# Kernel tuning notes

Hardware: AMD Instinct MI355X
Metric: run time of the kernel (lower is better)

Reference implementation:

```python
import jax, jax.numpy as jnp
import numpy as np

HEADS = 16

def split_heads(v, heads):
    # NOTE: faithful to the source: reshape [B,S,D] -> [B,S,h_dim,heads], then
    # transpose to [B,heads,S,h_dim]. This interleaves channels across heads
    # (different from the standard [B,S,heads,h_dim] split).
    B, S, D = v.shape
    hd = D // heads
    return v.reshape(B, S, hd, heads).transpose(0, 3, 1, 2)

def merge_heads(v):
    # [B,heads,S,h_dim] -> transpose [B,S,h_dim,heads] -> reshape [B,S,D]
    B, H, S, hd = v.shape
    return v.transpose(0, 2, 3, 1).reshape(B, S, H * hd)

def setup_inputs() -> dict:
    key = jax.random.key(0)
    ks = jax.random.split(key, 5)
    B, S, D = 2, 2048, 1024
    return {
        "x": jax.random.normal(ks[0], (B, S, D), dtype=jnp.float32),
        "qw": jax.random.normal(ks[1], (D, D), dtype=jnp.float32),
        "kw": jax.random.normal(ks[2], (D, D), dtype=jnp.float32),
        "vw": jax.random.normal(ks[3], (D, D), dtype=jnp.float32),
        "ow": jax.random.normal(ks[4], (D, D), dtype=jnp.float32),
    }

def reference(x, qw, kw, vw, ow):
    B, S, D = x.shape
    Q = split_heads(x @ qw, HEADS)  # [B,H,S,hd]
    K = split_heads(x @ kw, HEADS)
    V = split_heads(x @ vw, HEADS)
    # NOTE: scale is 1/sqrt(dim), NOT 1/sqrt(head_dim), as in the source.
    scale = 1.0 / jnp.sqrt(jnp.float32(D))
    score = jnp.einsum("bhqd,bhkd->bhqk", Q, K) * scale  # [B,H,S,S]
    causal = jnp.tril(jnp.ones((1, 1, S, S), dtype=score.dtype))
    score = score - 1e10 * (1.0 - causal)
    weights = jax.nn.softmax(score, axis=-1)
    attn = jnp.einsum("bhqk,bhkd->bhqd", weights, V)
    return merge_heads(attn) @ ow
```

## Files before the change

kernel.cpp:

```cpp
#include <hip/hip_runtime.h>


typedef __bf16 bf16x8 __attribute__((ext_vector_type(8)));
typedef float  f32x4  __attribute__((ext_vector_type(4)));

#define S_LEN  2048
#define DMODEL 1024
#define NHEADS 16
#define HDIM   64
#define LOG2E  1.44269504088896340736f

__device__ __forceinline__ void gll16(const __bf16* g, __bf16* l) {
    __builtin_amdgcn_global_load_lds(
        (const __attribute__((address_space(1))) unsigned int*)g,
        (__attribute__((address_space(3))) unsigned int*)l, 16, 0, 0);
}

__global__ __launch_bounds__(256) void prep_all(
    const float* __restrict__ x,
    const float* __restrict__ qw, const float* __restrict__ kw,
    const float* __restrict__ vw, const float* __restrict__ ow,
    __bf16* __restrict__ xhi, __bf16* __restrict__ xlo,
    __bf16* __restrict__ qwthi, __bf16* __restrict__ qwtlo,
    __bf16* __restrict__ kwthi, __bf16* __restrict__ kwtlo,
    __bf16* __restrict__ vwt,  __bf16* __restrict__ owt) {
    __shared__ float tile[32][33];
    int id = blockIdx.x;
    if (id < 4096) {
        int i = id * 256 + threadIdx.x;
        float4 v = ((const float4*)x)[i];
        __bf16 h0 = (__bf16)v.x, h1 = (__bf16)v.y, h2 = (__bf16)v.z, h3 = (__bf16)v.w;
        ushort4 hh, ll;
        hh.x = __builtin_bit_cast(unsigned short, h0);
        hh.y = __builtin_bit_cast(unsigned short, h1);
        hh.z = __builtin_bit_cast(unsigned short, h2);
        hh.w = __builtin_bit_cast(unsigned short, h3);
        ll.x = __builtin_bit_cast(unsigned short, (__bf16)(v.x - (float)h0));
        ll.y = __builtin_bit_cast(unsigned short, (__bf16)(v.y - (float)h1));
        ll.z = __builtin_bit_cast(unsigned short, (__bf16)(v.z - (float)h2));
        ll.w = __builtin_bit_cast(unsigned short, (__bf16)(v.w - (float)h3));
        ((ushort4*)xhi)[i] = hh;
        ((ushort4*)xlo)[i] = ll;
        return;
    }
    int rid = id - 4096;
    int z = rid >> 10;
    int bx = rid & 31, by = (rid >> 5) & 31;
    const float* w = (z == 0) ? qw : (z == 1) ? kw : (z == 2) ? vw : ow;
    int n0 = bx * 32, k0 = by * 32;
    int tx = threadIdx.x & 31, ty = threadIdx.x >> 5;
#pragma unroll
    for (int i = 0; i < 32; i += 8)
        tile[ty + i][tx] = w[(k0 + ty + i) * DMODEL + n0 + tx];
    __syncthreads();
#pragma unroll
    for (int i = 0; i < 32; i += 8) {
        float f = tile[tx][ty + i];
        int k = k0 + tx, n = n0 + ty + i;
        if (z <= 1) {
            __bf16 fh = (__bf16)f;
            __bf16 fl = (__bf16)(f - (float)fh);
            int c = (n & 15) * 64 + (n >> 4);
            if (z == 0) { qwthi[c * DMODEL + k] = fh; qwtlo[c * DMODEL + k] = fl; }
            else        { kwthi[c * DMODEL + k] = fh; kwtlo[c * DMODEL + k] = fl; }
        } else if (z == 2) {
            vwt[n * DMODEL + k] = (__bf16)f;
        } else {
            int ck = (k & 15) * 64 + (k >> 4);
            owt[n * DMODEL + ck] = (__bf16)f;
        }
    }
}

__global__ __launch_bounds__(256) void qkv_gemm(
    const __bf16* __restrict__ xhi, const __bf16* __restrict__ xlo,
    const __bf16* __restrict__ qwthi, const __bf16* __restrict__ qwtlo,
    const __bf16* __restrict__ kwthi, const __bf16* __restrict__ kwtlo,
    const __bf16* __restrict__ vwt,
    __bf16* __restrict__ Qhi, __bf16* __restrict__ Qlo,
    __bf16* __restrict__ Khi, __bf16* __restrict__ Klo,
    __bf16* __restrict__ Vt) {
    __shared__ __bf16 Ash[128][32], Asl[128][32], Bsh[128][32], Bsl[128][32];
    int mode = blockIdx.z;
    int tid  = threadIdx.x;
    int wave = tid >> 6, lane = tid & 63;
    int quad = lane >> 4, l15 = lane & 15;
    int wm = (wave >> 1) * 64, wn = (wave & 1) * 64;
    int grow = lane >> 2;
    int gcol = (((lane & 3) - ((lane >> 3) & 3)) & 3) * 8;
    int sA   = ((quad + (l15 >> 1)) & 3) * 8;
    const int K = DMODEL;

    if (mode < 2) {
        const __bf16* Bh = mode ? kwthi : qwthi;
        const __bf16* Bl = mode ? kwtlo : qwtlo;
        int m0 = blockIdx.y * 128, n0 = blockIdx.x * 128;
        f32x4 acc[4][4] = {};
        for (int k0 = 0; k0 < K; k0 += 32) {
            __syncthreads();
#pragma unroll
            for (int ps = 0; ps < 2; ps++) {
                int row = ps * 64 + wave * 16;
                gll16(&xhi[(m0 + row + grow) * K + k0 + gcol], &Ash[row][0]);
                gll16(&xlo[(m0 + row + grow) * K + k0 + gcol], &Asl[row][0]);
                gll16(&Bh [(n0 + row + grow) * K + k0 + gcol], &Bsh[row][0]);
                gll16(&Bl [(n0 + row + grow) * K + k0 + gcol], &Bsl[row][0]);
            }
            __syncthreads();
            bf16x8 ah[4], al[4], bh[4], bl[4];
#pragma unroll
            for (int mi = 0; mi < 4; mi++) {
                ah[mi] = *(const bf16x8*)&Ash[wm + mi * 16 + l15][sA];
                al[mi] = *(const bf16x8*)&Asl[wm + mi * 16 + l15][sA];
            }
#pragma unroll
            for (int ni = 0; ni < 4; ni++) {
                bh[ni] = *(const bf16x8*)&Bsh[wn + ni * 16 + l15][sA];
                bl[ni] = *(const bf16x8*)&Bsl[wn + ni * 16 + l15][sA];
            }
#pragma unroll
            for (int mi = 0; mi < 4; mi++)
#pragma unroll
                for (int ni = 0; ni < 4; ni++) {
                    acc[mi][ni] = __builtin_amdgcn_mfma_f32_16x16x32_bf16(ah[mi], bh[ni], acc[mi][ni], 0, 0, 0);
                    acc[mi][ni] = __builtin_amdgcn_mfma_f32_16x16x32_bf16(ah[mi], bl[ni], acc[mi][ni], 0, 0, 0);
                    acc[mi][ni] = __builtin_amdgcn_mfma_f32_16x16x32_bf16(al[mi], bh[ni], acc[mi][ni], 0, 0, 0);
                }
        }
        float oscale = mode ? 1.0f : 0.03125f * LOG2E;
        __bf16* Ohi = mode ? Khi : Qhi;
        __bf16* Olo = mode ? Klo : Qlo;
#pragma unroll
        for (int mi = 0; mi < 4; mi++)
#pragma unroll
            for (int ni = 0; ni < 4; ni++)
#pragma unroll
                for (int rg = 0; rg < 4; rg++) {
                    int m = m0 + wm + mi * 16 + quad * 4 + rg;
                    int n = n0 + wn + ni * 16 + l15;
                    float v = acc[mi][ni][rg] * oscale;
                    size_t idx = (size_t)m * DMODEL + n;
                    __bf16 vh = (__bf16)v;
                    Ohi[idx] = vh;
                    Olo[idx] = (__bf16)(v - (float)vh);
                }
    } else {
        int ch0 = blockIdx.x * 128, xm0 = blockIdx.y * 128;
        f32x4 acc[4][4] = {};
        for (int k0 = 0; k0 < K; k0 += 32) {
            __syncthreads();
#pragma unroll
            for (int ps = 0; ps < 2; ps++) {
                int row = ps * 64 + wave * 16;
                gll16(&vwt[(ch0 + row + grow) * K + k0 + gcol], &Ash[row][0]);
                gll16(&xhi[(xm0 + row + grow) * K + k0 + gcol], &Bsh[row][0]);
            }
            __syncthreads();
            bf16x8 af[4], bfr[4];
#pragma unroll
            for (int mi = 0; mi < 4; mi++)
                af[mi] = *(const bf16x8*)&Ash[wm + mi * 16 + l15][sA];
#pragma unroll
            for (int ni = 0; ni < 4; ni++)
                bfr[ni] = *(const bf16x8*)&Bsh[wn + ni * 16 + l15][sA];
#pragma unroll
            for (int mi = 0; mi < 4; mi++)
#pragma unroll
                for (int ni = 0; ni < 4; ni++)
                    acc[mi][ni] = __builtin_amdgcn_mfma_f32_16x16x32_bf16(
                        af[mi], bfr[ni], acc[mi][ni], 0, 0, 0);
        }
#pragma unroll
        for (int mi = 0; mi < 4; mi++)
#pragma unroll
            for (int ni = 0; ni < 4; ni++)
#pragma unroll
                for (int rg = 0; rg < 4; rg++) {
                    int ch = ch0 + wm + mi * 16 + quad * 4 + rg;
                    int xm = xm0 + wn + ni * 16 + l15;
                    int b = xm >> 11, s = xm & 2047;
                    int h = ch & 15,  d = ch >> 4;
                    Vt[((size_t)(b * NHEADS + h) * HDIM + d) * S_LEN + s] =
                        (__bf16)acc[mi][ni][rg];
                }
    }
}

__global__ __launch_bounds__(256) void out_gemm(const __bf16* __restrict__ A,
                                                const __bf16* __restrict__ Bt,
                                                float* __restrict__ out) {
    __shared__ __bf16 As[64][32];
    __shared__ __bf16 Bs[128][32];
    int tid  = threadIdx.x;
    int wave = tid >> 6, lane = tid & 63;
    int quad = lane >> 4, l15 = lane & 15;
    int m0 = blockIdx.y * 64, n0 = blockIdx.x * 128;
    int wm = (wave >> 1) * 32, wn = (wave & 1) * 64;
    int grow = lane >> 2;
    int gcol = (((lane & 3) - ((lane >> 3) & 3)) & 3) * 8;
    int sA   = ((quad + (l15 >> 1)) & 3) * 8;
    const int K = DMODEL;
    f32x4 acc[2][4] = {};

    for (int k0 = 0; k0 < K; k0 += 32) {
        __syncthreads();
        gll16(&A[(m0 + wave * 16 + grow) * K + k0 + gcol], &As[wave * 16][0]);
#pragma unroll
        for (int ps = 0; ps < 2; ps++) {
            int row = ps * 64 + wave * 16;
            gll16(&Bt[(n0 + row + grow) * K + k0 + gcol], &Bs[row][0]);
        }
        __syncthreads();
        bf16x8 af[2], bfr[4];
#pragma unroll
        for (int mi = 0; mi < 2; mi++)
            af[mi] = *(const bf16x8*)&As[wm + mi * 16 + l15][sA];
#pragma unroll
        for (int ni = 0; ni < 4; ni++)
            bfr[ni] = *(const bf16x8*)&Bs[wn + ni * 16 + l15][sA];
#pragma unroll
        for (int mi = 0; mi < 2; mi++)
#pragma unroll
            for (int ni = 0; ni < 4; ni++)
                acc[mi][ni] = __builtin_amdgcn_mfma_f32_16x16x32_bf16(
                    af[mi], bfr[ni], acc[mi][ni], 0, 0, 0);
    }

#pragma unroll
    for (int mi = 0; mi < 2; mi++)
#pragma unroll
        for (int ni = 0; ni < 4; ni++)
#pragma unroll
            for (int rg = 0; rg < 4; rg++) {
                int m = m0 + wm + mi * 16 + quad * 4 + rg;
                int n = n0 + wn + ni * 16 + l15;
                out[(size_t)m * DMODEL + n] = acc[mi][ni][rg];
            }
}

__global__ __launch_bounds__(256, 2) void flash_attn(const __bf16* __restrict__ Qhi,
                                                     const __bf16* __restrict__ Qlo,
                                                     const __bf16* __restrict__ Khi,
                                                     const __bf16* __restrict__ Klo,
                                                     const __bf16* __restrict__ Vt,
                                                     __bf16* __restrict__ attn) {
    int id  = blockIdx.x;
    int xcd = id & 7, r = id >> 3;
    int bh  = xcd + 8 * (r & 3);
    int rr  = r >> 2;
    int t   = (rr < 8) ? (15 - rr) : (rr - 8);
    int b = bh >> 4, h = bh & 15;
    const __bf16* Qh_hi = Qhi + (size_t)b * S_LEN * DMODEL + h * HDIM;
    const __bf16* Qh_lo = Qlo + (size_t)b * S_LEN * DMODEL + h * HDIM;
    const __bf16* Kh_hi = Khi + (size_t)b * S_LEN * DMODEL + h * HDIM;
    const __bf16* Kh_lo = Klo + (size_t)b * S_LEN * DMODEL + h * HDIM;
    const __bf16* Vh    = Vt  + (size_t)bh * HDIM * S_LEN;

    int tid = threadIdx.x, wave = tid >> 6, lane = tid & 63;
    int quad = lane >> 4, l15 = lane & 15;
    int iters = 2 * t + 2;

    __shared__ __bf16 KhF[8 * 64 * 8];
    __shared__ __bf16 KlF[8 * 64 * 8];
    __shared__ __bf16 VF [8 * 64 * 8];
    __shared__ __bf16 Ps[4][32][72];

    int c1  = tid >> 6, key = tid & 63;
    int inner = (c1 * 16 + (key & 15)) * 8;
    int rK    = (key >> 4);
    int kdst0 = rK * 512 + inner, kdst1 = (4 + rK) * 512 + inner;
    const __bf16* vrow = Vh + (size_t)key * S_LEN;

    int qbase = t * 128 + wave * 32;
    bf16x8 aqh0[2], aqh1[2], aql0[2], aql1[2];
#pragma unroll
    for (int qh = 0; qh < 2; qh++) {
        size_t qr = (size_t)(qbase + qh * 16 + l15) * DMODEL;
        aqh0[qh] = *(const bf16x8*)&Qh_hi[qr + quad * 8];
        aqh1[qh] = *(const bf16x8*)&Qh_hi[qr + 32 + quad * 8];
        aql0[qh] = *(const bf16x8*)&Qh_lo[qr + quad * 8];
        aql1[qh] = *(const bf16x8*)&Qh_lo[qr + 32 + quad * 8];
    }

    bf16x8 ones;
#pragma unroll
    for (int j = 0; j < 8; j++) ones[j] = (__bf16)1.0f;

    uint4 pk0, pk1, pl0, pl1, pv0, pv1;
    {
        const __bf16* sk = Kh_hi + (size_t)key * DMODEL;
        const __bf16* sl = Kh_lo + (size_t)key * DMODEL;
        pk0 = *(const uint4*)(sk + c1 * 8); pk1 = *(const uint4*)(sk + c1 * 8 + 32);
        pl0 = *(const uint4*)(sl + c1 * 8); pl1 = *(const uint4*)(sl + c1 * 8 + 32);
        pv0 = *(const uint4*)(vrow + c1 * 8); pv1 = *(const uint4*)(vrow + c1 * 8 + 32);
    }

    float m[2][4] = {{-3e38f, -3e38f, -3e38f, -3e38f},
                     {-3e38f, -3e38f, -3e38f, -3e38f}};
    f32x4 o[2][4] = {};
    f32x4 ol[2] = {};

    for (int i = 0; i < iters; i++) {
        int key0 = i * 64;

        __syncthreads();
        *(uint4*)&KhF[kdst0] = pk0;  *(uint4*)&KhF[kdst1] = pk1;
        *(uint4*)&KlF[kdst0] = pl0;  *(uint4*)&KlF[kdst1] = pl1;
        *(uint4*)&VF [kdst0] = pv0;  *(uint4*)&VF [kdst1] = pv1;
        __syncthreads();

        if (i + 1 < iters) {
            int key0n = (i + 1) * 64;
            const __bf16* sk = Kh_hi + (size_t)(key0n + key) * DMODEL;
            const __bf16* sl = Kh_lo + (size_t)(key0n + key) * DMODEL;
            pk0 = *(const uint4*)(sk + c1 * 8); pk1 = *(const uint4*)(sk + c1 * 8 + 32);
            pl0 = *(const uint4*)(sl + c1 * 8); pl1 = *(const uint4*)(sl + c1 * 8 + 32);
            pv0 = *(const uint4*)(vrow + key0n + c1 * 8);
            pv1 = *(const uint4*)(vrow + key0n + c1 * 8 + 32);
        }

        if (key0 > qbase + 31) continue;

        f32x4 sc[2][4] = {};
#pragma unroll
        for (int ni = 0; ni < 4; ni++) {
            bf16x8 kh0 = *(const bf16x8*)&KhF[(ni * 64 + lane) * 8];
            bf16x8 kh1 = *(const bf16x8*)&KhF[((4 + ni) * 64 + lane) * 8];
            bf16x8 kl0 = *(const bf16x8*)&KlF[(ni * 64 + lane) * 8];
            bf16x8 kl1 = *(const bf16x8*)&KlF[((4 + ni) * 64 + lane) * 8];
#pragma unroll
            for (int qh = 0; qh < 2; qh++) {
                sc[qh][ni] = __builtin_amdgcn_mfma_f32_16x16x32_bf16(aqh0[qh], kh0, sc[qh][ni], 0, 0, 0);
                sc[qh][ni] = __builtin_amdgcn_mfma_f32_16x16x32_bf16(aqh1[qh], kh1, sc[qh][ni], 0, 0, 0);
                sc[qh][ni] = __builtin_amdgcn_mfma_f32_16x16x32_bf16(aqh0[qh], kl0, sc[qh][ni], 0, 0, 0);
                sc[qh][ni] = __builtin_amdgcn_mfma_f32_16x16x32_bf16(aqh1[qh], kl1, sc[qh][ni], 0, 0, 0);
                sc[qh][ni] = __builtin_amdgcn_mfma_f32_16x16x32_bf16(aql0[qh], kh0, sc[qh][ni], 0, 0, 0);
                sc[qh][ni] = __builtin_amdgcn_mfma_f32_16x16x32_bf16(aql1[qh], kh1, sc[qh][ni], 0, 0, 0);
            }
        }

        if (i >= 2 * t) {
#pragma unroll
            for (int qh = 0; qh < 2; qh++) {
                int qrb = qbase + qh * 16 + quad * 4;
#pragma unroll
                for (int ni = 0; ni < 4; ni++) {
                    int keyi = key0 + ni * 16 + l15;
#pragma unroll
                    for (int rg = 0; rg < 4; rg++)
                        if (keyi > qrb + rg) sc[qh][ni][rg] = -1e30f;
                }
            }
        }

#pragma unroll
        for (int qh = 0; qh < 2; qh++) {
#pragma unroll
            for (int rg = 0; rg < 4; rg++) {
                float mx = fmaxf(fmaxf(sc[qh][0][rg], sc[qh][1][rg]),
                                 fmaxf(sc[qh][2][rg], sc[qh][3][rg]));
#pragma unroll
                for (int mm = 1; mm < 16; mm <<= 1)
                    mx = fmaxf(mx, __shfl_xor(mx, mm, 64));
                float mnew  = fmaxf(m[qh][rg], mx);
                float alpha = __builtin_amdgcn_exp2f(m[qh][rg] - mnew);
                m[qh][rg] = mnew;
#pragma unroll
                for (int ni = 0; ni < 4; ni++) {
                    float px = __builtin_amdgcn_exp2f(sc[qh][ni][rg] - mnew);
                    Ps[wave][qh * 16 + quad * 4 + rg][ni * 16 + l15] = (__bf16)px;
                }
                ol[qh][rg] *= alpha;
#pragma unroll
                for (int ni = 0; ni < 4; ni++)
                    o[qh][ni][rg] *= alpha;
            }
        }

#pragma unroll
        for (int step = 0; step < 2; step++) {
            bf16x8 ap0 = *(const bf16x8*)&Ps[wave][l15][step * 32 + quad * 8];
            bf16x8 ap1 = *(const bf16x8*)&Ps[wave][16 + l15][step * 32 + quad * 8];
            ol[0] = __builtin_amdgcn_mfma_f32_16x16x32_bf16(ap0, ones, ol[0], 0, 0, 0);
            ol[1] = __builtin_amdgcn_mfma_f32_16x16x32_bf16(ap1, ones, ol[1], 0, 0, 0);
#pragma unroll
            for (int ni = 0; ni < 4; ni++) {
                bf16x8 bv = *(const bf16x8*)&VF[((step * 4 + ni) * 64 + lane) * 8];
                o[0][ni] = __builtin_amdgcn_mfma_f32_16x16x32_bf16(ap0, bv, o[0][ni], 0, 0, 0);
                o[1][ni] = __builtin_amdgcn_mfma_f32_16x16x32_bf16(ap1, bv, o[1][ni], 0, 0, 0);
            }
        }
    }

#pragma unroll
    for (int qh = 0; qh < 2; qh++)
#pragma unroll
        for (int rg = 0; rg < 4; rg++) {
            float inv = 1.0f / ol[qh][rg];
            int q = qbase + qh * 16 + quad * 4 + rg;
#pragma unroll
            for (int ni = 0; ni < 4; ni++) {
                attn[((size_t)b * S_LEN + q) * DMODEL + h * HDIM + ni * 16 + l15] =
                    (__bf16)(o[qh][ni][rg] * inv);
            }
        }
}

extern "C" void kernel_launch(void* const* d_in, const int* in_sizes, int n_in,
                              void* d_out, int out_size, void* d_ws, size_t ws_size,
                              hipStream_t stream) {
    const float* x  = (const float*)d_in[0];
    const float* qw = (const float*)d_in[1];
    const float* kw = (const float*)d_in[2];
    const float* vw = (const float*)d_in[3];
    const float* ow = (const float*)d_in[4];

    char* ws = (char*)d_ws;
    const size_t MB = 1024 * 1024;
    __bf16* xhi   = (__bf16*)(ws);
    __bf16* xlo   = (__bf16*)(ws + 8 * MB);
    __bf16* qwthi = (__bf16*)(ws + 16 * MB);
    __bf16* qwtlo = (__bf16*)(ws + 18 * MB);
    __bf16* kwthi = (__bf16*)(ws + 20 * MB);
    __bf16* kwtlo = (__bf16*)(ws + 22 * MB);
    __bf16* vwt   = (__bf16*)(ws + 24 * MB);
    __bf16* owt   = (__bf16*)(ws + 26 * MB);
    __bf16* Qhi_b = (__bf16*)(ws + 28 * MB);
    __bf16* Qlo_b = (__bf16*)(ws + 36 * MB);
    __bf16* Khi_b = (__bf16*)(ws + 44 * MB);
    __bf16* Klo_b = (__bf16*)(ws + 52 * MB);
    __bf16* Vtb   = (__bf16*)(ws + 60 * MB);
    __bf16* attnb = xlo;

    prep_all<<<8192, 256, 0, stream>>>(x, qw, kw, vw, ow,
                                       xhi, xlo, qwthi, qwtlo, kwthi, kwtlo,
                                       vwt, owt);

    qkv_gemm<<<dim3(8, 32, 3), 256, 0, stream>>>(
        xhi, xlo, qwthi, qwtlo, kwthi, kwtlo, vwt,
        Qhi_b, Qlo_b, Khi_b, Klo_b, Vtb);

    flash_attn<<<512, 256, 0, stream>>>(Qhi_b, Qlo_b, Khi_b, Klo_b, Vtb, attnb);

    out_gemm<<<dim3(8, 64), 256, 0, stream>>>(attnb, owt, (float*)d_out);
}
```

Baseline: 259.9 us.

## Split attention key range across two blocks and merge with combine kernel

Each 128-query tile of the flash attention kernel is now handled by two blocks. Each block processes half of the causal key range and writes unnormalized bf16 partial outputs plus its row max and row sum to workspace. A new combine kernel rescales and merges the two partials into the final attention output. The aim is more parallelism, with the launch-bounds occupancy target raised from 2 to 3. In exchange it adds an extra kernel launch, workspace traffic for the partials, bf16 rounding of unnormalized partials, and uneven block lengths from the new tile ordering.

Result: no change. 258.1 us (-0.7%).

```diff
diff --git a/kernel.cpp b/kernel.cpp
--- a/kernel.cpp
+++ b/kernel.cpp
@@ -238,17 +238,22 @@
             }
 }
 
-__global__ __launch_bounds__(256, 2) void flash_attn(const __bf16* __restrict__ Qhi,
+__global__ __launch_bounds__(256, 3) void flash_attn(const __bf16* __restrict__ Qhi,
                                                      const __bf16* __restrict__ Qlo,
                                                      const __bf16* __restrict__ Khi,
                                                      const __bf16* __restrict__ Klo,
                                                      const __bf16* __restrict__ Vt,
-                                                     __bf16* __restrict__ attn) {
+                                                     __bf16* __restrict__ po0,
+                                                     __bf16* __restrict__ po1,
+                                                     float* __restrict__ pml) {
     int id  = blockIdx.x;
     int xcd = id & 7, r = id >> 3;
     int bh  = xcd + 8 * (r & 3);
     int rr  = r >> 2;
-    int t   = (rr < 8) ? (15 - rr) : (rr - 8);
+    int t   = 15 - (rr >> 1);
+    int half = rr & 1;
+    int i0 = half ? (t + 1) : 0;
+    int i1 = half ? (2 * t + 2) : (t + 1);
     int b = bh >> 4, h = bh & 15;
     const __bf16* Qh_hi = Qhi + (size_t)b * S_LEN * DMODEL + h * HDIM;
     const __bf16* Qh_lo = Qlo + (size_t)b * S_LEN * DMODEL + h * HDIM;
@@ -258,7 +263,6 @@
 
     int tid = threadIdx.x, wave = tid >> 6, lane = tid & 63;
     int quad = lane >> 4, l15 = lane & 15;
-    int iters = 2 * t + 2;
 
     __shared__ __bf16 KhF[8 * 64 * 8];
     __shared__ __bf16 KlF[8 * 64 * 8];
@@ -288,11 +292,12 @@
 
     uint4 pk0, pk1, pl0, pl1, pv0, pv1;
     {
-        const __bf16* sk = Kh_hi + (size_t)key * DMODEL;
-        const __bf16* sl = Kh_lo + (size_t)key * DMODEL;
+        const __bf16* sk = Kh_hi + (size_t)(i0 * 64 + key) * DMODEL;
+        const __bf16* sl = Kh_lo + (size_t)(i0 * 64 + key) * DMODEL;
         pk0 = *(const uint4*)(sk + c1 * 8); pk1 = *(const uint4*)(sk + c1 * 8 + 32);
         pl0 = *(const uint4*)(sl + c1 * 8); pl1 = *(const uint4*)(sl + c1 * 8 + 32);
-        pv0 = *(const uint4*)(vrow + c1 * 8); pv1 = *(const uint4*)(vrow + c1 * 8 + 32);
+        pv0 = *(const uint4*)(vrow + i0 * 64 + c1 * 8);
+        pv1 = *(const uint4*)(vrow + i0 * 64 + c1 * 8 + 32);
     }
 
     float m[2][4] = {{-3e38f, -3e38f, -3e38f, -3e38f},
@@ -300,7 +305,7 @@
     f32x4 o[2][4] = {};
     f32x4 ol[2] = {};
 
-    for (int i = 0; i < iters; i++) {
+    for (int i = i0; i < i1; i++) {
         int key0 = i * 64;
 
         __syncthreads();
@@ -309,7 +314,7 @@
         *(uint4*)&VF [kdst0] = pv0;  *(uint4*)&VF [kdst1] = pv1;
         __syncthreads();
 
-        if (i + 1 < iters) {
+        if (i + 1 < i1) {
             int key0n = (i + 1) * 64;
             const __bf16* sk = Kh_hi + (size_t)(key0n + key) * DMODEL;
             const __bf16* sl = Kh_lo + (size_t)(key0n + key) * DMODEL;
@@ -392,18 +397,60 @@
         }
     }
 
+    int pslot = bh * 16 + t;
+    __bf16* po = half ? po1 : po0;
+    float* pm = pml + ((size_t)half * 512 + pslot) * 256;
 #pragma unroll
     for (int qh = 0; qh < 2; qh++)
 #pragma unroll
         for (int rg = 0; rg < 4; rg++) {
-            float inv = 1.0f / ol[qh][rg];
-            int q = qbase + qh * 16 + quad * 4 + rg;
-#pragma unroll
-            for (int ni = 0; ni < 4; ni++) {
-                attn[((size_t)b * S_LEN + q) * DMODEL + h * HDIM + ni * 16 + l15] =
-                    (__bf16)(o[qh][ni][rg] * inv);
-            }
-        }
+            int row = wave * 32 + qh * 16 + quad * 4 + rg;
+            if (l15 == 0) { pm[row] = m[qh][rg]; pm[128 + row] = ol[qh][rg]; }
+#pragma unroll
+            for (int ni = 0; ni < 4; ni++)
+                po[((size_t)pslot * 128 + row) * 64 + ni * 16 + l15] =
+                    (__bf16)o[qh][ni][rg];
+        }
+}
+
+__global__ __launch_bounds__(256) void combine(const __bf16* __restrict__ po0,
+                                               const __bf16* __restrict__ po1,
+                                               const float* __restrict__ pml,
+                                               __bf16* __restrict__ attn) {
+    int bid = blockIdx.x;
+    int pslot = bid >> 1;
+    int bh = pslot >> 4, t = pslot & 15;
+    int b = bh >> 4, h = bh & 15;
+    int tid = threadIdx.x;
+    int row = (bid & 1) * 64 + (tid >> 2);
+    int c = (tid & 3) * 16;
+
+    const float* pm0 = pml + (size_t)pslot * 256;
+    const float* pm1 = pml + (size_t)(512 + pslot) * 256;
+    float m0 = pm0[row], l0 = pm0[128 + row];
+    float m1 = pm1[row], l1 = pm1[128 + row];
+    float mm = fmaxf(m0, m1);
+    float s0 = __builtin_amdgcn_exp2f(m0 - mm);
+    float s1 = __builtin_amdgcn_exp2f(m1 - mm);
+    float inv = 1.0f / (l0 * s0 + l1 * s1);
+    float w0 = s0 * inv, w1 = s1 * inv;
+
+    const __bf16* r0 = po0 + ((size_t)pslot * 128 + row) * 64 + c;
+    const __bf16* r1 = po1 + ((size_t)pslot * 128 + row) * 64 + c;
+    int q = t * 128 + row;
+    __bf16* dst = attn + ((size_t)b * S_LEN + q) * DMODEL + h * HDIM + c;
+    bf16x8 a0 = *(const bf16x8*)(r0);
+    bf16x8 a1 = *(const bf16x8*)(r0 + 8);
+    bf16x8 b0 = *(const bf16x8*)(r1);
+    bf16x8 b1 = *(const bf16x8*)(r1 + 8);
+    bf16x8 d0, d1;
+#pragma unroll
+    for (int e = 0; e < 8; e++) {
+        d0[e] = (__bf16)((float)a0[e] * w0 + (float)b0[e] * w1);
+        d1[e] = (__bf16)((float)a1[e] * w0 + (float)b1[e] * w1);
+    }
+    *(bf16x8*)(dst)     = d0;
+    *(bf16x8*)(dst + 8) = d1;
 }
 
 extern "C" void kernel_launch(void* const* d_in, const int* in_sizes, int n_in,
@@ -431,6 +478,9 @@
     __bf16* Klo_b = (__bf16*)(ws + 52 * MB);
     __bf16* Vtb   = (__bf16*)(ws + 60 * MB);
     __bf16* attnb = xlo;
+    __bf16* po0 = (__bf16*)(ws);
+    __bf16* po1 = (__bf16*)(ws + 16 * MB);
+    float*  pml = (float*)(ws + 24 * MB);
 
     prep_all<<<8192, 256, 0, stream>>>(x, qw, kw, vw, ow,
                                        xhi, xlo, qwthi, qwtlo, kwthi, kwtlo,
@@ -440,7 +490,10 @@
         xhi, xlo, qwthi, qwtlo, kwthi, kwtlo, vwt,
         Qhi_b, Qlo_b, Khi_b, Klo_b, Vtb);
 
-    flash_attn<<<512, 256, 0, stream>>>(Qhi_b, Qlo_b, Khi_b, Klo_b, Vtb, attnb);
+    flash_attn<<<1024, 256, 0, stream>>>(Qhi_b, Qlo_b, Khi_b, Klo_b, Vtb,
+                                         po0, po1, pml);
+
+    combine<<<1024, 256, 0, stream>>>(po0, po1, pml, attnb);
 
     out_gemm<<<dim3(8, 64), 256, 0, stream>>>(attnb, owt, (float*)d_out);
 }
```
